# Kernel optimization log

Hardware: AMD Instinct MI355X
Metric: run time of the kernel (lower is better)

Reference implementation:

```python
import jax, jax.numpy as jnp
import numpy as np

B, S, V, E, H, NL, NM = 32, 4096, 256, 128, 256, 3, 16


def setup_inputs() -> dict:
    key = jax.random.key(0)
    ks = jax.random.split(key, 8)
    return {
        "x": jax.random.randint(ks[0], (B, S), 0, V),
        "emb": jax.random.normal(ks[1], (V, E), jnp.float32) * 0.02,
        "W0": jax.random.normal(ks[2], (2 * H, E), jnp.float32) / np.sqrt(E).astype(np.float32),
        "b0": jnp.zeros((2 * H,), jnp.float32),
        "Wl": jax.random.normal(ks[3], (NL - 1, 2 * H, H), jnp.float32) / np.sqrt(H).astype(np.float32),
        "bl": jnp.zeros((NL - 1, 2 * H), jnp.float32),
        "Walign": jax.random.normal(ks[4], (H, E), jnp.float32) / np.sqrt(E).astype(np.float32),
        "Wout": jax.random.normal(ks[5], (V, H), jnp.float32) / np.sqrt(H).astype(np.float32),
        "bout": jnp.zeros((V,), jnp.float32),
        "num_memorize": NM,
    }


def _log_g(x):
    # log of g(x) = x + 0.5 for x >= 0, sigmoid(x) otherwise
    return jnp.where(x >= 0, jnp.log(jax.nn.relu(x) + 0.5), -jax.nn.softplus(-x))


def _mingru_scan(gate, hid):
    # Heinsen log-space parallel scan of h_t = (1-z_t) h_{t-1} + z_t g(hid_t),
    # z_t = sigmoid(gate_t), h_0 = g(0) = 0.5.  gate/hid: [B,S,H]
    log_z = -jax.nn.softplus(-gate)          # log sigmoid(gate)
    log_coeffs = -jax.nn.softplus(gate)      # log(1 - z)
    log_h0 = jnp.full(gate[:, :1].shape, jnp.log(0.5).astype(gate.dtype), gate.dtype)
    a_star = jnp.cumsum(jnp.pad(log_coeffs, ((0, 0), (1, 0), (0, 0))), axis=1)  # [B,S+1,H]
    log_vals = jnp.concatenate([log_h0, log_z + _log_g(hid)], axis=1)           # [B,S+1,H]
    h = jnp.exp(a_star + jax.lax.cumlogsumexp(log_vals - a_star, axis=1))
    return h[:, 1:]  # [B,S,H]


def reference(x, emb, W0, b0, Wl, bl, Walign, Wout, bout, num_memorize):
    h_in = emb[x]  # [B,S,E]
    # layer 0 (input dims E -> H, residual via alignment projection)
    gh = jnp.einsum('bse,ge->bsg', h_in, W0) + b0
    gate, hid = jnp.split(gh, 2, axis=-1)
    h = _mingru_scan(gate, hid) + jnp.einsum('bse,he->bsh', h_in, Walign)
    # layers 1..NL-1 (H -> H, identity residual)
    for i in range(Wl.shape[0]):
        gh = jnp.einsum('bsh,gh->bsg', h, Wl[i]) + bl[i]
        gate, hid = jnp.split(gh, 2, axis=-1)
        h = _mingru_scan(gate, hid) + h
    logits = jnp.einsum('bsh,vh->bsv', h, Wout) + bout  # [B,S,V]
    return logits[:, -num_memorize:]
```

## Files before the change

### kernel.cpp

```cpp
#include <hip/hip_runtime.h>
#include <hip/hip_bf16.h>

using bf16 = __hip_bfloat16;

constexpr int B_ = 32, S_ = 4096, V_ = 256, E_ = 128, H_ = 256, NM_ = 16;
constexpr int GH = 2 * H_;
constexpr int NC = 128, L_ = 32;

typedef __attribute__((ext_vector_type(8))) short bf16x8;
typedef __attribute__((ext_vector_type(4))) float f32x4;

__device__ __forceinline__ float b2f(unsigned short u) {
  union { float f; unsigned int i; } x; x.i = ((unsigned int)u) << 16; return x.f;
}
__device__ __forceinline__ unsigned short f2b(float f) {
  unsigned int i = __builtin_bit_cast(unsigned int, f);
  return (unsigned short)((i + 0x7fffu + ((i >> 16) & 1u)) >> 16);
}

__device__ __forceinline__ void step_ab(float gate, float hid, float& a, float& bt) {
  const float LOG2E = 1.4426950408889634f;
  float e  = __builtin_amdgcn_exp2f(gate * LOG2E);
  a = __builtin_amdgcn_rcpf(1.0f + e);
  float sn = __builtin_amdgcn_rcpf(1.0f + __builtin_amdgcn_exp2f(-hid * LOG2E));
  float g  = (hid >= 0.0f) ? (hid + 0.5f) : sn;
  bt = (1.0f - a) * g;
}

#define ATS(row, bcol) (((row) << 9) | ((bcol) ^ (((row) & 7) << 4)))


__global__ __launch_bounds__(256) void build_tables(
    const float* __restrict__ emb, const float* __restrict__ W0,
    const float* __restrict__ b0, const float* __restrict__ Walign,
    const float* __restrict__ Wl, float* __restrict__ T0, bf16* __restrict__ Wpk) {
  const int v = blockIdx.x;
  const int t = threadIdx.x;
  __shared__ float e[E_];
  if (t < E_) e[t] = emb[v * E_ + t];
  __syncthreads();
  const float4* w0g = (const float4*)(W0 + (size_t)t * E_);
  const float4* w0h = (const float4*)(W0 + (size_t)(t + 256) * E_);
  const float4* wal = (const float4*)(Walign + (size_t)t * E_);
  float g = b0[t], hd = b0[t + 256], al = 0.0f;
  #pragma unroll 8
  for (int k = 0; k < E_ / 4; ++k) {
    float4 ev = *(const float4*)(e + 4 * k);
    float4 ga = w0g[k]; g  += ga.x * ev.x + ga.y * ev.y + ga.z * ev.z + ga.w * ev.w;
    float4 hb = w0h[k]; hd += hb.x * ev.x + hb.y * ev.y + hb.z * ev.z + hb.w * ev.w;
    float4 aw = wal[k]; al += aw.x * ev.x + aw.y * ev.y + aw.z * ev.z + aw.w * ev.w;
  }
  float a, btv; step_ab(g, hd, a, btv);
  T0[(size_t)v * 768 + t]       = a;
  T0[(size_t)v * 768 + 256 + t] = btv;
  T0[(size_t)v * 768 + 512 + t] = al;

  const int fid = v * 256 + t;
  if (fid < 32768) {
    const int layer = fid >> 14;
    const int kk   = (fid >> 11) & 7;
    const int grp  = (fid >> 6) & 31;
    const int lane = fid & 63;
    const int row = grp * 16 + (lane & 15);
    const int k0  = kk * 32 + (lane >> 4) * 8;
    const float* src = Wl + (((size_t)layer * 512 + row) * 256 + k0);
    bf16* dst = Wpk + (size_t)fid * 8;
    #pragma unroll
    for (int e2 = 0; e2 < 8; ++e2) dst[e2] = __float2bfloat16(src[e2]);
  }
}

__global__ __launch_bounds__(256) void scanA_l0(const int* __restrict__ x, const float* __restrict__ T0,
                                                float* __restrict__ cAB) {
  const int b = blockIdx.y;
  const int wv = threadIdx.x >> 6, lane = threadIdx.x & 63;
  const int c = blockIdx.x * 4 + wv;
  const int t4 = lane * 4;
  const int* xp = x + (size_t)b * S_ + (size_t)c * L_;
  float A0=1,A1=1,A2=1,A3=1, B0=0,B1=0,B2=0,B3=0;
  #pragma unroll 4
  for (int t = 0; t < L_; ++t) {
    const float* tp = T0 + (size_t)xp[t] * 768;
    float4 a4 = *(const float4*)(tp + t4);
    float4 b4 = *(const float4*)(tp + 256 + t4);
    A0 = a4.x*A0; B0 = a4.x*B0 + b4.x;
    A1 = a4.y*A1; B1 = a4.y*B1 + b4.y;
    A2 = a4.z*A2; B2 = a4.z*B2 + b4.z;
    A3 = a4.w*A3; B3 = a4.w*B3 + b4.w;
  }
  float* o = cAB + (size_t)(b * NC + c) * 2 * H_;
  *(float4*)(o + t4)      = make_float4(A0, A1, A2, A3);
  *(float4*)(o + H_ + t4) = make_float4(B0, B1, B2, B3);
}

__global__ __launch_bounds__(256) void scanB(const float* __restrict__ cAB, float* __restrict__ cHin) {
  const int b = blockIdx.x, ch = threadIdx.x;
  const float* base = cAB + (size_t)b * NC * 2 * H_ + ch;
  float* out = cHin + (size_t)b * NC * H_ + ch;
  float a[8], bb[8], an[8], bn[8];
  #pragma unroll
  for (int i = 0; i < 8; ++i) { a[i] = base[(size_t)i * 2 * H_]; bb[i] = base[(size_t)i * 2 * H_ + H_]; }
  float hp = 0.5f;
  for (int tile = 0; tile < NC / 8; ++tile) {
    if (tile < NC / 8 - 1) {
      const float* nb = base + (size_t)(tile + 1) * 8 * 2 * H_;
      #pragma unroll
      for (int i = 0; i < 8; ++i) { an[i] = nb[(size_t)i * 2 * H_]; bn[i] = nb[(size_t)i * 2 * H_ + H_]; }
    }
    #pragma unroll
    for (int i = 0; i < 8; ++i) {
      out[(size_t)(tile * 8 + i) * H_] = hp;
      hp = a[i] * hp + bb[i];
    }
    #pragma unroll
    for (int i = 0; i < 8; ++i) { a[i] = an[i]; bb[i] = bn[i]; }
  }
}

__global__ __launch_bounds__(256) void scanC_l0(const int* __restrict__ x, const float* __restrict__ T0,
                                                const float* __restrict__ cHin, bf16* __restrict__ h) {
  const int b = blockIdx.y;
  const int wv = threadIdx.x >> 6, lane = threadIdx.x & 63;
  const int c = blockIdx.x * 4 + wv;
  const int t4 = lane * 4;
  float4 hr = *(const float4*)(cHin + ((size_t)b * NC + c) * H_ + t4);
  const int* xp = x + (size_t)b * S_ + (size_t)c * L_;
  unsigned short* hp = (unsigned short*)(h + ((size_t)b * S_ + (size_t)c * L_) * H_);
  #pragma unroll 4
  for (int t = 0; t < L_; ++t) {
    const float* tp = T0 + (size_t)xp[t] * 768;
    float4 a4 = *(const float4*)(tp + t4);
    float4 b4 = *(const float4*)(tp + 256 + t4);
    float4 r4 = *(const float4*)(tp + 512 + t4);
    hr.x = a4.x*hr.x + b4.x;
    hr.y = a4.y*hr.y + b4.y;
    hr.z = a4.z*hr.z + b4.z;
    hr.w = a4.w*hr.w + b4.w;
    ushort4 o;
    o.x = f2b(hr.x + r4.x);
    o.y = f2b(hr.y + r4.y);
    o.z = f2b(hr.z + r4.z);
    o.w = f2b(hr.w + r4.w);
    *(ushort4*)(hp + t4) = o;
    hp += H_;
  }
}

__device__ __forceinline__ void gemm_tile(const char* smem, const bf16* __restrict__ Wp,
                                          int lane, int wave,
                                          f32x4 (&accG)[2][4], f32x4 (&accH)[2][4]) {
  const int l15 = lane & 15, lhi = lane >> 4;
  #pragma unroll
  for (int kk = 0; kk < 8; ++kk) {
    const int kb = kk * 64 + lhi * 16;
    bf16x8 af[2], bG[4], bH[4];
    #pragma unroll
    for (int ni = 0; ni < 4; ++ni) {
      bG[ni] = *(const bf16x8*)(Wp + ((size_t)(kk * 2048 + (wave * 4 + ni) * 64 + lane)) * 8);
      bH[ni] = *(const bf16x8*)(Wp + ((size_t)(kk * 2048 + (16 + wave * 4 + ni) * 64 + lane)) * 8);
    }
    #pragma unroll
    for (int mi = 0; mi < 2; ++mi) {
      const int r = mi * 16 + l15;
      af[mi] = *(const bf16x8*)(smem + ATS(r, kb));
    }
    #pragma unroll
    for (int mi = 0; mi < 2; ++mi)
      #pragma unroll
      for (int ni = 0; ni < 4; ++ni) {
        accG[mi][ni] = __builtin_amdgcn_mfma_f32_16x16x32_bf16(af[mi], bG[ni], accG[mi][ni], 0, 0, 0);
        accH[mi][ni] = __builtin_amdgcn_mfma_f32_16x16x32_bf16(af[mi], bH[ni], accH[mi][ni], 0, 0, 0);
      }
  }
}

__device__ __forceinline__ void epilogue_fold(
    const f32x4 (&accG)[2][4], const f32x4 (&accH)[2][4],
    const float* __restrict__ bias, int lane, int wave,
    const char* __restrict__ smemA,
    const float (&h0m1v)[4],
    unsigned int* __restrict__ scr,
    uint4* __restrict__ ghc4, bool doStore,
    float* __restrict__ o) {
  const int l15 = lane & 15, lhi = lane >> 4;
  #pragma unroll
  for (int ni = 0; ni < 4; ++ni) {
    const int colG = wave * 64 + ni * 16 + l15;
    const float bg = bias[colG], bh = bias[colG + 256];
    float segA[2], segB[2];
    #pragma unroll
    for (int mi = 0; mi < 2; ++mi) {
      const int r0 = mi * 16 + lhi * 4;
      float hprev = (r0 == 0) ? h0m1v[ni]
                  : b2f(*(const unsigned short*)(smemA + ATS(r0 - 1, colG * 2)));
      float Aa = 1.0f, Bb = 0.0f;
      unsigned int pk[4];
      #pragma unroll
      for (int j = 0; j < 4; ++j) {
        float a, btv;
        step_ab(accG[mi][ni][j] + bg, accH[mi][ni][j] + bh, a, btv);
        float hcurr = b2f(*(const unsigned short*)(smemA + ATS(r0 + j, colG * 2)));
        float bp = btv + hcurr - a * hprev;
        hprev = hcurr;
        const unsigned short ua = f2b(a), ub = f2b(bp);
        pk[j] = ((unsigned int)ua << 16) | ub;
        const float ar = b2f(ua), br = b2f(ub);
        Aa = ar * Aa; Bb = ar * Bb + br;
      }
      if (doStore) {
        unsigned int* wp = scr + l15 * 32 + (((mi * 16 + lhi * 4)) ^ ((l15 & 7) << 2));
        *(uint4*)wp = make_uint4(pk[0], pk[1], pk[2], pk[3]);
      }
      segA[mi] = Aa; segB[mi] = Bb;
    }
    if (doStore) {
      #pragma unroll
      for (int s = 0; s < 2; ++s) {
        const int lin = s * 64 + lane;
        const int ch = lin >> 3, uq = lin & 7;
        uint4 v = *(const uint4*)(scr + ch * 32 + ((uq * 4) ^ ((ch & 7) << 2)));
        ghc4[(size_t)(wave * 64 + ni * 16) * 8 + lin] = v;
      }
    }
    #pragma unroll
    for (int mi = 0; mi < 2; ++mi) {
      float A = segA[mi], Bv = segB[mi];
      {
        float Ap = __shfl_xor(A, 16), Bp = __shfl_xor(Bv, 16);
        float Bn = (lhi & 1) ? (A * Bp + Bv) : (Ap * Bv + Bp);
        A = A * Ap; Bv = Bn;
      }
      {
        float Ap = __shfl_xor(A, 32), Bp = __shfl_xor(Bv, 32);
        float Bn = (lhi & 2) ? (A * Bp + Bv) : (Ap * Bv + Bp);
        A = A * Ap; Bv = Bn;
      }
      segA[mi] = A; segB[mi] = Bv;
    }
    const float Ac = segA[1] * segA[0];
    const float Bc = segA[1] * segB[0] + segB[1];
    if (lhi == 0) { o[colG] = Ac; o[H_ + colG] = Bc; }
  }
}

__global__ __launch_bounds__(256, 4) void gemm_scanA(
    const bf16* __restrict__ Ain, const bf16* __restrict__ Wp,
    const float* __restrict__ bias, unsigned int* __restrict__ gh2,
    float* __restrict__ cAB) {
  __shared__ __align__(16) char smem[24576];
  const int bid = blockIdx.x;
  const int c = bid & (NC - 1), b = bid >> 7;
  const size_t row0 = (size_t)b * S_ + (size_t)c * L_;
  const int tid = threadIdx.x, lane = tid & 63, wave = tid >> 6;
  const int l15 = lane & 15;

  const char* Ag = (const char*)(Ain + row0 * 256);
  #pragma unroll
  for (int it = 0; it < 4; ++it) {
    const int o = it * 4096 + tid * 16;
    const int row = o >> 9, bb = o & 511;
    const int src = (row << 9) | (bb ^ ((row & 7) << 4));
    char* lbase = smem + it * 4096 + wave * 1024;
    __builtin_amdgcn_global_load_lds((const __attribute__((address_space(1))) void*)(Ag + src),
                                     (__attribute__((address_space(3))) void*)lbase, 16, 0, 0);
  }
  float h0m1v[4];
  #pragma unroll
  for (int ni = 0; ni < 4; ++ni) {
    const int colG = wave * 64 + ni * 16 + l15;
    h0m1v[ni] = (c > 0) ? b2f(((const unsigned short*)Ain)[(row0 - 1) * 256 + colG]) : 0.0f;
  }
  __syncthreads();

  f32x4 accG[2][4] = {}, accH[2][4] = {};
  gemm_tile(smem, Wp, lane, wave, accG, accH);
  unsigned int* scr = (unsigned int*)(smem + 16384) + wave * 512;
  uint4* ghc4 = (uint4*)(gh2 + ((size_t)b * NC + c) * (L_ * 256));
  epilogue_fold(accG, accH, bias, lane, wave, smem, h0m1v, scr, ghc4, true,
                cAB + ((size_t)b * NC + c) * 2 * H_);
}

__global__ __launch_bounds__(256, 4) void scan_gemm(
    unsigned int* __restrict__ gh2, const float* __restrict__ cHin,
    const bf16* __restrict__ Wp, const float* __restrict__ bias,
    float* __restrict__ cAB) {
  __shared__ __align__(16) char smem[24576];
  const int bid = blockIdx.x;
  const int c = bid & (NC - 1), b = bid >> 7;
  const int tid = threadIdx.x, lane = tid & 63, wave = tid >> 6;
  const int l15 = lane & 15;
  const int ch = tid;

  float hp = cHin[((size_t)b * NC + c) * H_ + ch];
  const uint4* pq = (const uint4*)(gh2 + ((size_t)b * NC + c) * (L_ * 256)) + ch * 8;
  #pragma unroll
  for (int tt = 0; tt < 8; ++tt) {
    uint4 v = pq[tt];
    hp = b2f(v.x >> 16) * hp + b2f(v.x & 0xffffu);
    *(unsigned short*)(smem + ATS(tt * 4 + 0, ch * 2)) = f2b(hp);
    hp = b2f(v.y >> 16) * hp + b2f(v.y & 0xffffu);
    *(unsigned short*)(smem + ATS(tt * 4 + 1, ch * 2)) = f2b(hp);
    hp = b2f(v.z >> 16) * hp + b2f(v.z & 0xffffu);
    *(unsigned short*)(smem + ATS(tt * 4 + 2, ch * 2)) = f2b(hp);
    hp = b2f(v.w >> 16) * hp + b2f(v.w & 0xffffu);
    *(unsigned short*)(smem + ATS(tt * 4 + 3, ch * 2)) = f2b(hp);
  }
  float h0m1v[4];
  #pragma unroll
  for (int ni = 0; ni < 4; ++ni) {
    const int colG = wave * 64 + ni * 16 + l15;
    h0m1v[ni] = cHin[((size_t)b * NC + c) * H_ + colG];
  }
  __syncthreads();

  f32x4 accG[2][4] = {}, accH[2][4] = {};
  gemm_tile(smem, Wp, lane, wave, accG, accH);
  unsigned int* scr = (unsigned int*)(smem + 16384) + wave * 512;
  uint4* ghc4 = (uint4*)(gh2 + ((size_t)b * NC + c) * (L_ * 256));
  epilogue_fold(accG, accH, bias, lane, wave, smem, h0m1v, scr, ghc4, c >= NC - 4,
                cAB + ((size_t)b * NC + c) * 2 * H_);
}

__global__ __launch_bounds__(256) void scanC_tail(const unsigned int* __restrict__ gh2,
                                                  const float* __restrict__ cHin,
                                                  bf16* __restrict__ h) {
  const int b = blockIdx.y;
  const int c = (NC - 4) + blockIdx.x;
  const int ch = threadIdx.x;
  const size_t row0 = (size_t)b * S_ + (size_t)c * L_;
  float hp = cHin[((size_t)b * NC + c) * H_ + ch];
  const uint4* pq = (const uint4*)(gh2 + ((size_t)b * NC + c) * (L_ * 256)) + ch * 8;
  unsigned short* hio = (unsigned short*)h + row0 * 256 + ch;
  #pragma unroll
  for (int tt = 0; tt < 8; ++tt) {
    uint4 v = pq[tt];
    hp = b2f(v.x >> 16) * hp + b2f(v.x & 0xffffu); hio[(tt * 4 + 0) * 256] = f2b(hp);
    hp = b2f(v.y >> 16) * hp + b2f(v.y & 0xffffu); hio[(tt * 4 + 1) * 256] = f2b(hp);
    hp = b2f(v.z >> 16) * hp + b2f(v.z & 0xffffu); hio[(tt * 4 + 2) * 256] = f2b(hp);
    hp = b2f(v.w >> 16) * hp + b2f(v.w & 0xffffu); hio[(tt * 4 + 3) * 256] = f2b(hp);
  }
}

__global__ __launch_bounds__(256) void out_logits(const bf16* __restrict__ h,
                                                  const float* __restrict__ Wout,
                                                  const float* __restrict__ bout,
                                                  float* __restrict__ out) {
  const int r = blockIdx.x;
  const int b = r >> 4, si = r & 15;
  const int v = threadIdx.x;
  __shared__ float hs[H_];
  const size_t t = (size_t)b * S_ + (S_ - NM_ + si);
  hs[v] = b2f(((const unsigned short*)h)[t * H_ + v]);
  __syncthreads();
  float acc = bout[v];
  const float4* w4 = (const float4*)(Wout + (size_t)v * H_);
  #pragma unroll 8
  for (int k = 0; k < H_ / 4; ++k) {
    float4 wv = w4[k];
    float4 hv = *(const float4*)(hs + 4 * k);
    acc += wv.x * hv.x + wv.y * hv.y + wv.z * hv.z + wv.w * hv.w;
  }
  out[(size_t)r * V_ + v] = acc;
}

extern "C" void kernel_launch(void* const* d_in, const int* in_sizes, int n_in,
                              void* d_out, int out_size, void* d_ws, size_t ws_size,
                              hipStream_t stream) {
  const int*   x      = (const int*)d_in[0];
  const float* emb    = (const float*)d_in[1];
  const float* W0     = (const float*)d_in[2];
  const float* b0     = (const float*)d_in[3];
  const float* Wl     = (const float*)d_in[4];
  const float* bl     = (const float*)d_in[5];
  const float* Walign = (const float*)d_in[6];
  const float* Wout   = (const float*)d_in[7];
  const float* bout   = (const float*)d_in[8];
  (void)in_sizes; (void)n_in; (void)out_size; (void)ws_size;

  char* ws = (char*)d_ws;
  size_t off = 0;
  unsigned int* gh2 = (unsigned int*)(ws + off); off += (size_t)B_ * S_ * 256 * 4;
  bf16*  h    = (bf16*)(ws + off);  off += (size_t)B_ * S_ * H_ * 2;
  float* cAB  = (float*)(ws + off); off += (size_t)B_ * NC * 2 * H_ * 4;
  float* cHin = (float*)(ws + off); off += (size_t)B_ * NC * H_ * 4;
  float* T0   = (float*)(ws + off); off += (size_t)V_ * 768 * 4;
  bf16*  Wpk  = (bf16*)(ws + off);  off += (size_t)2 * GH * H_ * 2;

  build_tables<<<256, 256, 0, stream>>>(emb, W0, b0, Walign, Wl, T0, Wpk);

  dim3 gscan(NC / 4, B_);
  scanA_l0<<<gscan, 256, 0, stream>>>(x, T0, cAB);
  scanB<<<B_, 256, 0, stream>>>(cAB, cHin);
  scanC_l0<<<gscan, 256, 0, stream>>>(x, T0, cHin, h);

  const bf16* Wpk2 = Wpk + (size_t)GH * H_;
  gemm_scanA<<<B_ * NC, 256, 0, stream>>>(h, Wpk, bl, gh2, cAB);
  scanB<<<B_, 256, 0, stream>>>(cAB, cHin);
  scan_gemm<<<B_ * NC, 256, 0, stream>>>(gh2, cHin, Wpk2, bl + GH, cAB);
  scanB<<<B_, 256, 0, stream>>>(cAB, cHin);
  scanC_tail<<<dim3(4, B_), 256, 0, stream>>>(gh2, cHin, h);

  out_logits<<<B_ * NM_, 256, 0, stream>>>(h, Wout, bout, (float*)d_out);
}
```

Baseline: 239.8 us.

## Fuse layer-0 scan completion into the first GEMM kernel, dropping the h round-trip

Removes the separate scanC_l0 kernel. The layer-0 recurrence now runs per chunk inside the first GEMM kernel, which writes bf16 activations straight into LDS instead of writing h to global memory and reloading it. The previous-row value is recomputed from the table, and the scratch space moves into separate shared arrays. Launch bounds go from 4 to 6 blocks per CU, and the tail scan shrinks to the final chunk only, since NM=16 fits inside the last 32-row chunk. The cost is a serial 32-step table walk inside the GEMM kernel and higher register and LDS pressure from the larger occupancy target.

```diff
diff --git a/kernel.cpp b/kernel.cpp
--- a/kernel.cpp
+++ b/kernel.cpp
@@ -117,35 +117,6 @@
   }
 }
 
-__global__ __launch_bounds__(256) void scanC_l0(const int* __restrict__ x, const float* __restrict__ T0,
-                                                const float* __restrict__ cHin, bf16* __restrict__ h) {
-  const int b = blockIdx.y;
-  const int wv = threadIdx.x >> 6, lane = threadIdx.x & 63;
-  const int c = blockIdx.x * 4 + wv;
-  const int t4 = lane * 4;
-  float4 hr = *(const float4*)(cHin + ((size_t)b * NC + c) * H_ + t4);
-  const int* xp = x + (size_t)b * S_ + (size_t)c * L_;
-  unsigned short* hp = (unsigned short*)(h + ((size_t)b * S_ + (size_t)c * L_) * H_);
-  #pragma unroll 4
-  for (int t = 0; t < L_; ++t) {
-    const float* tp = T0 + (size_t)xp[t] * 768;
-    float4 a4 = *(const float4*)(tp + t4);
-    float4 b4 = *(const float4*)(tp + 256 + t4);
-    float4 r4 = *(const float4*)(tp + 512 + t4);
-    hr.x = a4.x*hr.x + b4.x;
-    hr.y = a4.y*hr.y + b4.y;
-    hr.z = a4.z*hr.z + b4.z;
-    hr.w = a4.w*hr.w + b4.w;
-    ushort4 o;
-    o.x = f2b(hr.x + r4.x);
-    o.y = f2b(hr.y + r4.y);
-    o.z = f2b(hr.z + r4.z);
-    o.w = f2b(hr.w + r4.w);
-    *(ushort4*)(hp + t4) = o;
-    hp += H_;
-  }
-}
-
 __device__ __forceinline__ void gemm_tile(const char* smem, const bf16* __restrict__ Wp,
                                           int lane, int wave,
                                           f32x4 (&accG)[2][4], f32x4 (&accH)[2][4]) {
@@ -178,7 +149,7 @@
     const f32x4 (&accG)[2][4], const f32x4 (&accH)[2][4],
     const float* __restrict__ bias, int lane, int wave,
     const char* __restrict__ smemA,
-    const float (&h0m1v)[4],
+    const float* __restrict__ hm1s,
     unsigned int* __restrict__ scr,
     uint4* __restrict__ ghc4, bool doStore,
     float* __restrict__ o) {
@@ -191,7 +162,7 @@
     #pragma unroll
     for (int mi = 0; mi < 2; ++mi) {
       const int r0 = mi * 16 + lhi * 4;
-      float hprev = (r0 == 0) ? h0m1v[ni]
+      float hprev = (r0 == 0) ? hm1s[colG]
                   : b2f(*(const unsigned short*)(smemA + ATS(r0 - 1, colG * 2)));
       float Aa = 1.0f, Bb = 0.0f;
       unsigned int pk[4];
@@ -243,55 +214,62 @@
   }
 }
 
-__global__ __launch_bounds__(256, 4) void gemm_scanA(
-    const bf16* __restrict__ Ain, const bf16* __restrict__ Wp,
-    const float* __restrict__ bias, unsigned int* __restrict__ gh2,
-    float* __restrict__ cAB) {
-  __shared__ __align__(16) char smem[24576];
+__global__ __launch_bounds__(256, 6) void l0_gemm_scanA(
+    const int* __restrict__ x, const float* __restrict__ T0,
+    const float* __restrict__ cHin0,
+    const bf16* __restrict__ Wp, const float* __restrict__ bias,
+    unsigned int* __restrict__ gh2, float* __restrict__ cAB) {
+  __shared__ __align__(16) char smem[16384];
+  __shared__ unsigned int scrs[4][512];
+  __shared__ float hm1s[256];
+  __shared__ int xs[32];
   const int bid = blockIdx.x;
   const int c = bid & (NC - 1), b = bid >> 7;
   const size_t row0 = (size_t)b * S_ + (size_t)c * L_;
   const int tid = threadIdx.x, lane = tid & 63, wave = tid >> 6;
-  const int l15 = lane & 15;
-
-  const char* Ag = (const char*)(Ain + row0 * 256);
-  #pragma unroll
-  for (int it = 0; it < 4; ++it) {
-    const int o = it * 4096 + tid * 16;
-    const int row = o >> 9, bb = o & 511;
-    const int src = (row << 9) | (bb ^ ((row & 7) << 4));
-    char* lbase = smem + it * 4096 + wave * 1024;
-    __builtin_amdgcn_global_load_lds((const __attribute__((address_space(1))) void*)(Ag + src),
-                                     (__attribute__((address_space(3))) void*)lbase, 16, 0, 0);
-  }
-  float h0m1v[4];
-  #pragma unroll
-  for (int ni = 0; ni < 4; ++ni) {
-    const int colG = wave * 64 + ni * 16 + l15;
-    h0m1v[ni] = (c > 0) ? b2f(((const unsigned short*)Ain)[(row0 - 1) * 256 + colG]) : 0.0f;
+  const int ch = tid;
+
+  if (tid < 32) xs[tid] = x[row0 + tid];
+  float state = cHin0[((size_t)b * NC + c) * H_ + ch];
+  {
+    float hm1 = 0.0f;
+    if (c > 0) {
+      const int xm1 = x[row0 - 1];
+      hm1 = b2f(f2b(state + T0[(size_t)xm1 * 768 + 512 + ch]));
+    }
+    hm1s[ch] = hm1;
+  }
+  __syncthreads();
+  #pragma unroll 8
+  for (int t = 0; t < L_; ++t) {
+    const float* tp = T0 + (size_t)xs[t] * 768;
+    float a = tp[ch], bt = tp[256 + ch], r = tp[512 + ch];
+    state = a * state + bt;
+    *(unsigned short*)(smem + ATS(t, ch * 2)) = f2b(state + r);
   }
   __syncthreads();
 
   f32x4 accG[2][4] = {}, accH[2][4] = {};
   gemm_tile(smem, Wp, lane, wave, accG, accH);
-  unsigned int* scr = (unsigned int*)(smem + 16384) + wave * 512;
   uint4* ghc4 = (uint4*)(gh2 + ((size_t)b * NC + c) * (L_ * 256));
-  epilogue_fold(accG, accH, bias, lane, wave, smem, h0m1v, scr, ghc4, true,
+  epilogue_fold(accG, accH, bias, lane, wave, smem, hm1s, scrs[wave], ghc4, true,
                 cAB + ((size_t)b * NC + c) * 2 * H_);
 }
 
-__global__ __launch_bounds__(256, 4) void scan_gemm(
+__global__ __launch_bounds__(256, 6) void scan_gemm(
     unsigned int* __restrict__ gh2, const float* __restrict__ cHin,
     const bf16* __restrict__ Wp, const float* __restrict__ bias,
     float* __restrict__ cAB) {
-  __shared__ __align__(16) char smem[24576];
+  __shared__ __align__(16) char smem[16384];
+  __shared__ unsigned int scrs[4][512];
+  __shared__ float hm1s[256];
   const int bid = blockIdx.x;
   const int c = bid & (NC - 1), b = bid >> 7;
   const int tid = threadIdx.x, lane = tid & 63, wave = tid >> 6;
-  const int l15 = lane & 15;
   const int ch = tid;
 
   float hp = cHin[((size_t)b * NC + c) * H_ + ch];
+  hm1s[ch] = hp;
   const uint4* pq = (const uint4*)(gh2 + ((size_t)b * NC + c) * (L_ * 256)) + ch * 8;
   #pragma unroll
   for (int tt = 0; tt < 8; ++tt) {
@@ -305,27 +283,20 @@
     hp = b2f(v.w >> 16) * hp + b2f(v.w & 0xffffu);
     *(unsigned short*)(smem + ATS(tt * 4 + 3, ch * 2)) = f2b(hp);
   }
-  float h0m1v[4];
-  #pragma unroll
-  for (int ni = 0; ni < 4; ++ni) {
-    const int colG = wave * 64 + ni * 16 + l15;
-    h0m1v[ni] = cHin[((size_t)b * NC + c) * H_ + colG];
-  }
   __syncthreads();
 
   f32x4 accG[2][4] = {}, accH[2][4] = {};
   gemm_tile(smem, Wp, lane, wave, accG, accH);
-  unsigned int* scr = (unsigned int*)(smem + 16384) + wave * 512;
   uint4* ghc4 = (uint4*)(gh2 + ((size_t)b * NC + c) * (L_ * 256));
-  epilogue_fold(accG, accH, bias, lane, wave, smem, h0m1v, scr, ghc4, c >= NC - 4,
+  epilogue_fold(accG, accH, bias, lane, wave, smem, hm1s, scrs[wave], ghc4, c >= NC - 1,
                 cAB + ((size_t)b * NC + c) * 2 * H_);
 }
 
 __global__ __launch_bounds__(256) void scanC_tail(const unsigned int* __restrict__ gh2,
                                                   const float* __restrict__ cHin,
                                                   bf16* __restrict__ h) {
-  const int b = blockIdx.y;
-  const int c = (NC - 4) + blockIdx.x;
+  const int b = blockIdx.x;
+  const int c = NC - 1;
   const int ch = threadIdx.x;
   const size_t row0 = (size_t)b * S_ + (size_t)c * L_;
   float hp = cHin[((size_t)b * NC + c) * H_ + ch];
@@ -391,14 +362,13 @@
   dim3 gscan(NC / 4, B_);
   scanA_l0<<<gscan, 256, 0, stream>>>(x, T0, cAB);
   scanB<<<B_, 256, 0, stream>>>(cAB, cHin);
-  scanC_l0<<<gscan, 256, 0, stream>>>(x, T0, cHin, h);
 
   const bf16* Wpk2 = Wpk + (size_t)GH * H_;
-  gemm_scanA<<<B_ * NC, 256, 0, stream>>>(h, Wpk, bl, gh2, cAB);
+  l0_gemm_scanA<<<B_ * NC, 256, 0, stream>>>(x, T0, cHin, Wpk, bl, gh2, cAB);
   scanB<<<B_, 256, 0, stream>>>(cAB, cHin);
   scan_gemm<<<B_ * NC, 256, 0, stream>>>(gh2, cHin, Wpk2, bl + GH, cAB);
   scanB<<<B_, 256, 0, stream>>>(cAB, cHin);
-  scanC_tail<<<dim3(4, B_), 256, 0, stream>>>(gh2, cHin, h);
+  scanC_tail<<<B_, 256, 0, stream>>>(gh2, cHin, h);
 
   out_logits<<<B_ * NM_, 256, 0, stream>>>(h, Wout, bout, (float*)d_out);
 }
```

After: 874.8 us. +264.8%, slower.
